# Kernel optimization log

Measured on AMD Instinct MI355X. Metric: run time of the kernel, lower is better.

The kernel has to match this reference:

```python
import jax, jax.numpy as jnp
import numpy as np

D_MODEL = 512
D_K = 64
D_V = 64
N_HEADS = 8
N = 4096
EPS = 1e-5


def setup_inputs() -> dict:
    key = jax.random.key(0)
    ks = jax.random.split(key, 12)
    s = 1.0 / np.sqrt(D_MODEL)
    return {
        "Q": jax.random.normal(ks[0], (N, D_MODEL), dtype=jnp.float32),
        "K": jax.random.normal(ks[1], (N, D_MODEL), dtype=jnp.float32),
        "V": jax.random.normal(ks[2], (N, D_MODEL), dtype=jnp.float32),
        "W_Q": jax.random.normal(ks[3], (D_K * N_HEADS, D_MODEL), dtype=jnp.float32) * s,
        "b_Q": jnp.zeros((D_K * N_HEADS,), jnp.float32),
        "W_K": jax.random.normal(ks[4], (D_K * N_HEADS, D_MODEL), dtype=jnp.float32) * s,
        "b_K": jnp.zeros((D_K * N_HEADS,), jnp.float32),
        "W_V": jax.random.normal(ks[5], (D_V * N_HEADS, D_MODEL), dtype=jnp.float32) * s,
        "b_V": jnp.zeros((D_V * N_HEADS,), jnp.float32),
        "W_O": jax.random.normal(ks[6], (D_MODEL, N_HEADS * D_V), dtype=jnp.float32) * s,
        "b_O": jnp.zeros((D_MODEL,), jnp.float32),
        "gamma": jnp.ones((D_MODEL,), jnp.float32),
        "beta": jnp.zeros((D_MODEL,), jnp.float32),
    }


def reference(Q, K, V, W_Q, b_Q, W_K, b_K, W_V, b_V, W_O, b_O, gamma, beta):
    n = Q.shape[0]
    # projections (torch Linear: x @ W.T + b), then split heads: [N, H, dk]
    Qs = (Q @ W_Q.T + b_Q).reshape(n, N_HEADS, D_K)
    Ks = (K @ W_K.T + b_K).reshape(n, N_HEADS, D_K)
    Vs = (V @ W_V.T + b_V).reshape(n, N_HEADS, D_V)
    # per-head scaled dot-product attention over the N dim, batched via einsum
    scores = jnp.einsum("nhd,mhd->hnm", Qs, Ks) / np.sqrt(D_K)  # [H, N, N]
    attn = jax.nn.softmax(scores, axis=-1)
    ctx = jnp.einsum("hnm,mhd->nhd", attn, Vs)  # [N, H, dv]
    context = ctx.reshape(n, N_HEADS * D_V)  # concat heads (matches torch.cat order)
    out = context @ W_O.T + b_O + Q  # output proj + residual
    # LayerNorm over last dim
    mu = jnp.mean(out, axis=-1, keepdims=True)
    var = jnp.mean((out - mu) ** 2, axis=-1, keepdims=True)
    return (out - mu) * jax.lax.rsqrt(var + EPS) * gamma + beta
```

## Files before the change

### kernel.cpp

```cpp
#include <hip/hip_runtime.h>
#include <cstdint>

#define N_TOK 4096
#define DMODEL 512
#define NHEADS 8
#define HDIM 64

typedef unsigned short u16;
typedef __bf16 bf16x8 __attribute__((ext_vector_type(8)));
typedef float f32x4 __attribute__((ext_vector_type(4)));

union U128 { uint4 u; bf16x8 b; u16 s[8]; };

__device__ __forceinline__ u16 f2bf(float f) {
  uint32_t u = __builtin_bit_cast(uint32_t, f);
  u += 0x7FFFu + ((u >> 16) & 1u);
  return (u16)(u >> 16);
}
__device__ __forceinline__ float bf2f(u16 s) {
  uint32_t u = ((uint32_t)s) << 16;
  return __builtin_bit_cast(float, u);
}
__device__ __forceinline__ uint32_t fbit(float f) { return __builtin_bit_cast(uint32_t, f); }

#if __has_builtin(__builtin_amdgcn_exp2f)
#define EXP2(x) __builtin_amdgcn_exp2f(x)
#else
#define EXP2(x) __expf((x) * 0.6931471805599453f)
#endif

__device__ __forceinline__ void ldg2lds16(const void* g, void* s) {
  __builtin_amdgcn_global_load_lds(
      (const __attribute__((address_space(1))) void*)g,
      (__attribute__((address_space(3))) void*)s, 16, 0, 0);
}

__global__ __launch_bounds__(256) void cvt7_kernel(
    const float* __restrict__ Q, const float* __restrict__ K, const float* __restrict__ V,
    const float* __restrict__ WQ, const float* __restrict__ WK, const float* __restrict__ WV,
    const float* __restrict__ WO,
    u16* __restrict__ Qb, u16* __restrict__ Kb, u16* __restrict__ Vb,
    u16* __restrict__ WQb, u16* __restrict__ WKb, u16* __restrict__ WVb,
    u16* __restrict__ WOb)
{
  int b = blockIdx.x;
  const float* src; u16* dst; int rel;
  if      (b < 2048) { src = Q;  dst = Qb;  rel = b; }
  else if (b < 4096) { src = K;  dst = Kb;  rel = b - 2048; }
  else if (b < 6144) { src = V;  dst = Vb;  rel = b - 4096; }
  else if (b < 6400) { src = WQ; dst = WQb; rel = b - 6144; }
  else if (b < 6656) { src = WK; dst = WKb; rel = b - 6400; }
  else if (b < 6912) { src = WV; dst = WVb; rel = b - 6656; }
  else               { src = WO; dst = WOb; rel = b - 6912; }
  int i = (rel * 256 + threadIdx.x) * 4;
  float4 f = *(const float4*)(src + i);
  ushort4 o;
  o.x = f2bf(f.x); o.y = f2bf(f.y); o.z = f2bf(f.z); o.w = f2bf(f.w);
  *(ushort4*)(dst + i) = o;
}

__global__ __launch_bounds__(256) void proj3_kernel(
    const u16* __restrict__ Qb, const u16* __restrict__ Kb, const u16* __restrict__ Vb,
    const u16* __restrict__ WQb, const u16* __restrict__ WKb, const u16* __restrict__ WVb,
    const float* __restrict__ bQ, const float* __restrict__ bK, const float* __restrict__ bV,
    u16* __restrict__ Qs, u16* __restrict__ Ks, u16* __restrict__ Vt)
{
  const int z = blockIdx.z;
  const u16* A      = (z == 0) ? Qb : (z == 1) ? Kb : Vb;
  const u16* W      = (z == 0) ? WQb : (z == 1) ? WKb : WVb;
  const float* bias = (z == 0) ? bQ : (z == 1) ? bK : bV;

  const int m0 = blockIdx.x * 128;
  const int j0 = blockIdx.y * 64;
  const int tid = threadIdx.x;
  const int w = tid >> 6, lane = tid & 63, quad = lane >> 4, l = lane & 15;

  __shared__ bf16x8 sA[2][8][128];
  __shared__ bf16x8 sB[2][8][64];

  const f32x4 zero = {0.f, 0.f, 0.f, 0.f};
  f32x4 acc[2][4];
#pragma unroll
  for (int m = 0; m < 2; ++m)
#pragma unroll
    for (int s = 0; s < 4; ++s) acc[m][s] = zero;

  auto stage = [&](int kt, int buf) {
    const int k0 = kt * 64;
#pragma unroll
    for (int i = 0; i < 4; ++i) {
      const int chunk = 2 * w + (i >> 1), half = (i & 1) * 64;
      const u16* ag = A + (size_t)(m0 + half + lane) * DMODEL + k0 + chunk * 8;
      ldg2lds16(ag, (char*)&sA[buf][chunk][half]);
    }
#pragma unroll
    for (int i = 0; i < 2; ++i) {
      const int chunk = 2 * w + i;
      const u16* bg = W + (size_t)(j0 + lane) * DMODEL + k0 + chunk * 8;
      ldg2lds16(bg, (char*)&sB[buf][chunk][0]);
    }
  };

  stage(0, 0);
  __syncthreads();
  for (int kt = 0; kt < 8; ++kt) {
    const int buf = kt & 1;
    if (kt + 1 < 8) stage(kt + 1, buf ^ 1);
#pragma unroll
    for (int c = 0; c < 2; ++c) {
      bf16x8 af0 = sA[buf][c * 4 + quad][w * 32 + l];
      bf16x8 af1 = sA[buf][c * 4 + quad][w * 32 + 16 + l];
#pragma unroll
      for (int s = 0; s < 4; ++s) {
        bf16x8 bfb = sB[buf][c * 4 + quad][s * 16 + l];
        acc[0][s] = __builtin_amdgcn_mfma_f32_16x16x32_bf16(af0, bfb, acc[0][s], 0, 0, 0);
        acc[1][s] = __builtin_amdgcn_mfma_f32_16x16x32_bf16(af1, bfb, acc[1][s], 0, 0, 0);
      }
    }
    __syncthreads();
  }

#pragma unroll
  for (int m = 0; m < 2; ++m)
#pragma unroll
    for (int s = 0; s < 4; ++s) {
      int j = j0 + s * 16 + l;
      float bv = bias[j];
      int n0 = m0 + w * 32 + m * 16 + quad * 4;
      if (z < 2) {
        u16* Y = (z == 0) ? Qs : Ks;
#pragma unroll
        for (int r = 0; r < 4; ++r)
          Y[(size_t)(n0 + r) * DMODEL + j] = f2bf(acc[m][s][r] + bv);
      } else {
        ushort4 pk;
        pk.x = f2bf(acc[m][s][0] + bv); pk.y = f2bf(acc[m][s][1] + bv);
        pk.z = f2bf(acc[m][s][2] + bv); pk.w = f2bf(acc[m][s][3] + bv);
        *(ushort4*)(Vt + (size_t)j * N_TOK + n0) = pk;
      }
    }
}

__global__ __launch_bounds__(512, 4) void attn_kernel(
    const u16* __restrict__ Qs, const u16* __restrict__ Ks,
    const u16* __restrict__ Vt, u16* __restrict__ Opart, float* __restrict__ Lpart)
{
  const int hs = blockIdx.x;
  const int h = hs & 7, split = hs >> 3;
  const int qt = blockIdx.y;
  const int tid = threadIdx.x;
  const int w = tid >> 6, lane = tid & 63, quad = lane >> 4, l = lane & 15;

  __shared__ bf16x8 kch[2][8][64];
  __shared__ bf16x8 vch[2][8][64];
  __shared__ __align__(16) u16 pbuf[8][32][40];

  const int wq0 = qt * 256 + w * 32;

  bf16x8 qf[2][2];
#pragma unroll
  for (int c = 0; c < 2; ++c)
#pragma unroll
    for (int m = 0; m < 2; ++m) {
      U128 u;
      u.u = *(const uint4*)(Qs + (size_t)(wq0 + m * 16 + l) * DMODEL + h * HDIM + c * 32 + quad * 8);
#pragma unroll
      for (int j = 0; j < 8; ++j) u.s[j] = f2bf(bf2f(u.s[j]) * 0.18033688f);
      qf[c][m] = u.b;
    }

  const f32x4 zero = {0.f, 0.f, 0.f, 0.f};
  f32x4 o[2][4];
  float lsum[2] = {0.f, 0.f};
#pragma unroll
  for (int m = 0; m < 2; ++m)
#pragma unroll
    for (int s = 0; s < 4; ++s) o[m][s] = zero;

  auto stage = [&](int it, int buf) {
    const int j0 = split * 1024 + it * 64;
    if (w < 4) {
      const u16* kg = Ks + (size_t)(j0 + lane) * DMODEL + h * HDIM + w * 16;
      ldg2lds16(kg,     (char*)&kch[buf][2 * w][0]);
      ldg2lds16(kg + 8, (char*)&kch[buf][2 * w + 1][0]);
    } else {
      const int w2 = w - 4;
      const u16* vg = Vt + (size_t)(h * HDIM + lane) * N_TOK + j0 + w2 * 16;
      ldg2lds16(vg,     (char*)&vch[buf][2 * w2][0]);
      ldg2lds16(vg + 8, (char*)&vch[buf][2 * w2 + 1][0]);
    }
  };

  stage(0, 0);
  __syncthreads();

  for (int it = 0; it < 16; ++it) {
    const int buf = it & 1;
    if (it + 1 < 16) stage(it + 1, buf ^ 1);

#pragma unroll
    for (int kh = 0; kh < 2; ++kh) {
#pragma unroll
      for (int tt = 0; tt < 2; ++tt) {
        const int t = kh * 2 + tt;
        f32x4 sacc[2];
        sacc[0] = zero; sacc[1] = zero;
#pragma unroll
        for (int c = 0; c < 2; ++c) {
          bf16x8 kf = kch[buf][c * 4 + quad][t * 16 + l];
          sacc[0] = __builtin_amdgcn_mfma_f32_16x16x32_bf16(kf, qf[c][0], sacc[0], 0, 0, 0);
          sacc[1] = __builtin_amdgcn_mfma_f32_16x16x32_bf16(kf, qf[c][1], sacc[1], 0, 0, 0);
        }
#pragma unroll
        for (int m = 0; m < 2; ++m) {
          float p0 = EXP2(sacc[m][0]);
          float p1 = EXP2(sacc[m][1]);
          float p2 = EXP2(sacc[m][2]);
          float p3 = EXP2(sacc[m][3]);
          lsum[m] += (p0 + p1) + (p2 + p3);
          uint2 st;
          st.x = (fbit(p0) >> 16) | (fbit(p1) & 0xFFFF0000u);
          st.y = (fbit(p2) >> 16) | (fbit(p3) & 0xFFFF0000u);
          *(uint2*)&pbuf[w][m * 16 + l][tt * 16 + quad * 4] = st;
        }
      }
      U128 pf0, pf1;
      pf0.u = *(const uint4*)&pbuf[w][l][quad * 8];
      pf1.u = *(const uint4*)&pbuf[w][16 + l][quad * 8];
#pragma unroll
      for (int s = 0; s < 4; ++s) {
        bf16x8 vf = vch[buf][kh * 4 + quad][s * 16 + l];
        o[0][s] = __builtin_amdgcn_mfma_f32_16x16x32_bf16(pf0.b, vf, o[0][s], 0, 0, 0);
        o[1][s] = __builtin_amdgcn_mfma_f32_16x16x32_bf16(pf1.b, vf, o[1][s], 0, 0, 0);
      }
    }
    __syncthreads();
  }

#pragma unroll
  for (int m = 0; m < 2; ++m) {
    lsum[m] += __shfl_xor(lsum[m], 16);
    lsum[m] += __shfl_xor(lsum[m], 32);
  }
  if (quad == 0) {
    Lpart[((size_t)split * NHEADS + h) * N_TOK + wq0 + l]      = lsum[0];
    Lpart[((size_t)split * NHEADS + h) * N_TOK + wq0 + 16 + l] = lsum[1];
  }
  u16* Ob = Opart + ((size_t)(split * NHEADS + h) * N_TOK + wq0) * 64;
#pragma unroll
  for (int m = 0; m < 2; ++m)
#pragma unroll
    for (int s = 0; s < 4; ++s)
#pragma unroll
      for (int r = 0; r < 4; ++r)
        Ob[(size_t)(m * 16 + quad * 4 + r) * 64 + s * 16 + l] = f2bf(o[m][s][r]);
}

__global__ __launch_bounds__(256) void combine_kernel(
    const u16* __restrict__ Opart, const float* __restrict__ Lpart,
    u16* __restrict__ ctx)
{
  int idx = blockIdx.x * 256 + threadIdx.x;
  int n = idx >> 6;
  int c8 = idx & 63;
  int h = c8 >> 3;
  int vd0 = (c8 & 7) * 8;

  float acc[8] = {0, 0, 0, 0, 0, 0, 0, 0};
  float lsum = 0.f;
#pragma unroll
  for (int s = 0; s < 4; ++s) {
    U128 u;
    u.u = *(const uint4*)(Opart + ((size_t)(s * NHEADS + h) * N_TOK + n) * 64 + vd0);
#pragma unroll
    for (int j = 0; j < 8; ++j) acc[j] += bf2f(u.s[j]);
    lsum += Lpart[((size_t)s * NHEADS + h) * N_TOK + n];
  }
  float inv = 1.f / lsum;
  U128 u;
#pragma unroll
  for (int j = 0; j < 8; ++j) u.s[j] = f2bf(acc[j] * inv);
  *(uint4*)(ctx + (size_t)n * DMODEL + h * HDIM + vd0) = u.u;
}

__global__ __launch_bounds__(256) void gemmo_kernel(
    const u16* __restrict__ ctx, const u16* __restrict__ WOb,
    const float* __restrict__ bO, const float* __restrict__ resid,
    float* __restrict__ Y)
{
  const int m0 = blockIdx.x * 64;
  const int j0 = blockIdx.y * 64;
  const int tid = threadIdx.x;
  const int w = tid >> 6, lane = tid & 63, quad = lane >> 4, l = lane & 15;

  __shared__ bf16x8 sA[2][8][64];
  __shared__ bf16x8 sB[2][8][64];

  const f32x4 zero = {0.f, 0.f, 0.f, 0.f};
  f32x4 acc[4];
#pragma unroll
  for (int s = 0; s < 4; ++s) acc[s] = zero;

  auto stage = [&](int kt, int buf) {
    const int k0 = kt * 64;
#pragma unroll
    for (int i = 0; i < 2; ++i) {
      const int chunk = 2 * w + i;
      const u16* ag = ctx + (size_t)(m0 + lane) * DMODEL + k0 + chunk * 8;
      ldg2lds16(ag, (char*)&sA[buf][chunk][0]);
      const u16* bg = WOb + (size_t)(j0 + lane) * DMODEL + k0 + chunk * 8;
      ldg2lds16(bg, (char*)&sB[buf][chunk][0]);
    }
  };

  stage(0, 0);
  __syncthreads();
  for (int kt = 0; kt < 8; ++kt) {
    const int buf = kt & 1;
    if (kt + 1 < 8) stage(kt + 1, buf ^ 1);
#pragma unroll
    for (int c = 0; c < 2; ++c) {
      bf16x8 af = sA[buf][c * 4 + quad][w * 16 + l];
#pragma unroll
      for (int s = 0; s < 4; ++s) {
        bf16x8 bfb = sB[buf][c * 4 + quad][s * 16 + l];
        acc[s] = __builtin_amdgcn_mfma_f32_16x16x32_bf16(af, bfb, acc[s], 0, 0, 0);
      }
    }
    __syncthreads();
  }
#pragma unroll
  for (int s = 0; s < 4; ++s) {
    int j = j0 + s * 16 + l;
    float bv = bO[j];
    int n0 = m0 + w * 16 + quad * 4;
#pragma unroll
    for (int r = 0; r < 4; ++r)
      Y[(size_t)(n0 + r) * DMODEL + j] = acc[s][r] + bv + resid[(size_t)(n0 + r) * DMODEL + j];
  }
}

__global__ __launch_bounds__(256) void ln_kernel(
    const float* __restrict__ X, const float* __restrict__ gamma,
    const float* __restrict__ beta, float* __restrict__ Y)
{
  const int w = threadIdx.x >> 6, lane = threadIdx.x & 63;
  const int row = blockIdx.x * 4 + w;
  const float* x = X + (size_t)row * DMODEL + lane * 8;
  float4 a = *(const float4*)x;
  float4 b = *(const float4*)(x + 4);

  float s = a.x + a.y + a.z + a.w + b.x + b.y + b.z + b.w;
#pragma unroll
  for (int m = 1; m < 64; m <<= 1) s += __shfl_xor(s, m);
  float mu = s * (1.f / DMODEL);

  float d0 = a.x - mu, d1 = a.y - mu, d2 = a.z - mu, d3 = a.w - mu;
  float d4 = b.x - mu, d5 = b.y - mu, d6 = b.z - mu, d7 = b.w - mu;
  float v = d0*d0 + d1*d1 + d2*d2 + d3*d3 + d4*d4 + d5*d5 + d6*d6 + d7*d7;
#pragma unroll
  for (int m = 1; m < 64; m <<= 1) v += __shfl_xor(v, m);
  float sc = rsqrtf(v * (1.f / DMODEL) + 1e-5f);

  const float* g = gamma + lane * 8;
  const float* be = beta + lane * 8;
  float4 go = *(const float4*)g;
  float4 g1 = *(const float4*)(g + 4);
  float4 bo = *(const float4*)be;
  float4 b1 = *(const float4*)(be + 4);

  float4 y0, y1;
  y0.x = d0 * sc * go.x + bo.x;  y0.y = d1 * sc * go.y + bo.y;
  y0.z = d2 * sc * go.z + bo.z;  y0.w = d3 * sc * go.w + bo.w;
  y1.x = d4 * sc * g1.x + b1.x;  y1.y = d5 * sc * g1.y + b1.y;
  y1.z = d6 * sc * g1.z + b1.z;  y1.w = d7 * sc * g1.w + b1.w;

  float* yp = Y + (size_t)row * DMODEL + lane * 8;
  *(float4*)yp = y0;
  *(float4*)(yp + 4) = y1;
}

extern "C" void kernel_launch(void* const* d_in, const int* in_sizes, int n_in,
                              void* d_out, int out_size, void* d_ws, size_t ws_size,
                              hipStream_t stream)
{
  const float* Q     = (const float*)d_in[0];
  const float* K     = (const float*)d_in[1];
  const float* V     = (const float*)d_in[2];
  const float* WQ    = (const float*)d_in[3];
  const float* bQ    = (const float*)d_in[4];
  const float* WK    = (const float*)d_in[5];
  const float* bK    = (const float*)d_in[6];
  const float* WV    = (const float*)d_in[7];
  const float* bV    = (const float*)d_in[8];
  const float* WO    = (const float*)d_in[9];
  const float* bO    = (const float*)d_in[10];
  const float* gamma = (const float*)d_in[11];
  const float* beta  = (const float*)d_in[12];

  const size_t MB = 1ull << 20;
  char* ws = (char*)d_ws;
  u16* Qb   = (u16*)(ws + 0 * MB);
  u16* Kb   = (u16*)(ws + 4 * MB);
  u16* Vb   = (u16*)(ws + 8 * MB);
  u16* WQb  = (u16*)(ws + 12 * MB);
  u16* WKb  = (u16*)(ws + 12 * MB + 512 * 1024);
  u16* WVb  = (u16*)(ws + 13 * MB);
  u16* WOb  = (u16*)(ws + 13 * MB + 512 * 1024);
  u16* Qs   = (u16*)(ws + 14 * MB);
  u16* Ks   = (u16*)(ws + 18 * MB);
  u16* Vt   = (u16*)(ws + 22 * MB);
  u16* ctx  = (u16*)(ws + 26 * MB);
  u16* Opart = (u16*)(ws + 30 * MB);
  float* tmp = (float*)(ws + 30 * MB);
  float* Lpart = (float*)(ws + 46 * MB);
  float* out = (float*)d_out;

  cvt7_kernel<<<7168, 256, 0, stream>>>(Q, K, V, WQ, WK, WV, WO,
                                        Qb, Kb, Vb, WQb, WKb, WVb, WOb);
  proj3_kernel<<<dim3(32, 8, 3), 256, 0, stream>>>(Qb, Kb, Vb, WQb, WKb, WVb,
                                                   bQ, bK, bV, Qs, Ks, Vt);
  attn_kernel<<<dim3(32, 16), 512, 0, stream>>>(Qs, Ks, Vt, Opart, Lpart);
  combine_kernel<<<1024, 256, 0, stream>>>(Opart, Lpart, ctx);
  gemmo_kernel<<<dim3(64, 8), 256, 0, stream>>>(ctx, WOb, bO, Q, tmp);
  ln_kernel<<<1024, 256, 0, stream>>>(tmp, gamma, beta, out);
}
```

Baseline: 181.0 us.

## Fuse split-KV combine and LayerNorm into producers via last-block atomic counters

Removes the separate combine and LayerNorm launches. The last attention block to finish for each (head, query-tile) reduces the four split partials into ctx, and the last output-projection block for each row tile applies LayerNorm to its 64 rows. Each handoff uses threadfence plus an atomic counter, with a memset added to reset the counters. This saves two launches and some global round-trips, but the reduction and LayerNorm tails now run serially on a few blocks while others idle.

```diff
diff --git a/kernel.cpp b/kernel.cpp
--- a/kernel.cpp
+++ b/kernel.cpp
@@ -143,7 +143,8 @@
 
 __global__ __launch_bounds__(512, 4) void attn_kernel(
     const u16* __restrict__ Qs, const u16* __restrict__ Ks,
-    const u16* __restrict__ Vt, u16* __restrict__ Opart, float* __restrict__ Lpart)
+    const u16* __restrict__ Vt, u16* __restrict__ Opart, float* __restrict__ Lpart,
+    u16* __restrict__ ctx, unsigned int* __restrict__ cnt)
 {
   const int hs = blockIdx.x;
   const int h = hs & 7, split = hs >> 3;
@@ -154,6 +155,7 @@
   __shared__ bf16x8 kch[2][8][64];
   __shared__ bf16x8 vch[2][8][64];
   __shared__ __align__(16) u16 pbuf[8][32][40];
+  __shared__ int lastflag;
 
   const int wq0 = qt * 256 + w * 32;
 
@@ -254,39 +256,47 @@
 #pragma unroll
       for (int r = 0; r < 4; ++r)
         Ob[(size_t)(m * 16 + quad * 4 + r) * 64 + s * 16 + l] = f2bf(o[m][s][r]);
-}
-
-__global__ __launch_bounds__(256) void combine_kernel(
-    const u16* __restrict__ Opart, const float* __restrict__ Lpart,
-    u16* __restrict__ ctx)
-{
-  int idx = blockIdx.x * 256 + threadIdx.x;
-  int n = idx >> 6;
-  int c8 = idx & 63;
-  int h = c8 >> 3;
-  int vd0 = (c8 & 7) * 8;
-
-  float acc[8] = {0, 0, 0, 0, 0, 0, 0, 0};
-  float lsum = 0.f;
-#pragma unroll
-  for (int s = 0; s < 4; ++s) {
-    U128 u;
-    u.u = *(const uint4*)(Opart + ((size_t)(s * NHEADS + h) * N_TOK + n) * 64 + vd0);
-#pragma unroll
-    for (int j = 0; j < 8; ++j) acc[j] += bf2f(u.s[j]);
-    lsum += Lpart[((size_t)s * NHEADS + h) * N_TOK + n];
-  }
-  float inv = 1.f / lsum;
-  U128 u;
-#pragma unroll
-  for (int j = 0; j < 8; ++j) u.s[j] = f2bf(acc[j] * inv);
-  *(uint4*)(ctx + (size_t)n * DMODEL + h * HDIM + vd0) = u.u;
+
+  __threadfence();
+  __syncthreads();
+  if (tid == 0) {
+    unsigned int old = atomicAdd(&cnt[h * 16 + qt], 1u);
+    lastflag = (old == 3u);
+  }
+  __syncthreads();
+  if (lastflag) {
+    __threadfence();
+#pragma unroll
+    for (int i = 0; i < 4; ++i) {
+      int flat = tid + 512 * i;
+      int q = flat >> 3;
+      int vd0 = (flat & 7) * 8;
+      int n = qt * 256 + q;
+      float acc[8] = {0, 0, 0, 0, 0, 0, 0, 0};
+      float ls = 0.f;
+#pragma unroll
+      for (int s = 0; s < 4; ++s) {
+        U128 u;
+        u.u = *(const uint4*)(Opart + ((size_t)(s * NHEADS + h) * N_TOK + n) * 64 + vd0);
+#pragma unroll
+        for (int j = 0; j < 8; ++j) acc[j] += bf2f(u.s[j]);
+        ls += Lpart[((size_t)s * NHEADS + h) * N_TOK + n];
+      }
+      float inv = 1.f / ls;
+      U128 o8;
+#pragma unroll
+      for (int j = 0; j < 8; ++j) o8.s[j] = f2bf(acc[j] * inv);
+      *(uint4*)(ctx + (size_t)n * DMODEL + h * HDIM + vd0) = o8.u;
+    }
+  }
 }
 
 __global__ __launch_bounds__(256) void gemmo_kernel(
     const u16* __restrict__ ctx, const u16* __restrict__ WOb,
     const float* __restrict__ bO, const float* __restrict__ resid,
-    float* __restrict__ Y)
+    float* __restrict__ Y,
+    const float* __restrict__ gamma, const float* __restrict__ beta,
+    float* __restrict__ out, unsigned int* __restrict__ cnt2)
 {
   const int m0 = blockIdx.x * 64;
   const int j0 = blockIdx.y * 64;
@@ -295,6 +305,7 @@
 
   __shared__ bf16x8 sA[2][8][64];
   __shared__ bf16x8 sB[2][8][64];
+  __shared__ int lastf;
 
   const f32x4 zero = {0.f, 0.f, 0.f, 0.f};
   f32x4 acc[4];
@@ -338,46 +349,52 @@
     for (int r = 0; r < 4; ++r)
       Y[(size_t)(n0 + r) * DMODEL + j] = acc[s][r] + bv + resid[(size_t)(n0 + r) * DMODEL + j];
   }
-}
-
-__global__ __launch_bounds__(256) void ln_kernel(
-    const float* __restrict__ X, const float* __restrict__ gamma,
-    const float* __restrict__ beta, float* __restrict__ Y)
-{
-  const int w = threadIdx.x >> 6, lane = threadIdx.x & 63;
-  const int row = blockIdx.x * 4 + w;
-  const float* x = X + (size_t)row * DMODEL + lane * 8;
-  float4 a = *(const float4*)x;
-  float4 b = *(const float4*)(x + 4);
-
-  float s = a.x + a.y + a.z + a.w + b.x + b.y + b.z + b.w;
-#pragma unroll
-  for (int m = 1; m < 64; m <<= 1) s += __shfl_xor(s, m);
-  float mu = s * (1.f / DMODEL);
-
-  float d0 = a.x - mu, d1 = a.y - mu, d2 = a.z - mu, d3 = a.w - mu;
-  float d4 = b.x - mu, d5 = b.y - mu, d6 = b.z - mu, d7 = b.w - mu;
-  float v = d0*d0 + d1*d1 + d2*d2 + d3*d3 + d4*d4 + d5*d5 + d6*d6 + d7*d7;
-#pragma unroll
-  for (int m = 1; m < 64; m <<= 1) v += __shfl_xor(v, m);
-  float sc = rsqrtf(v * (1.f / DMODEL) + 1e-5f);
-
-  const float* g = gamma + lane * 8;
-  const float* be = beta + lane * 8;
-  float4 go = *(const float4*)g;
-  float4 g1 = *(const float4*)(g + 4);
-  float4 bo = *(const float4*)be;
-  float4 b1 = *(const float4*)(be + 4);
-
-  float4 y0, y1;
-  y0.x = d0 * sc * go.x + bo.x;  y0.y = d1 * sc * go.y + bo.y;
-  y0.z = d2 * sc * go.z + bo.z;  y0.w = d3 * sc * go.w + bo.w;
-  y1.x = d4 * sc * g1.x + b1.x;  y1.y = d5 * sc * g1.y + b1.y;
-  y1.z = d6 * sc * g1.z + b1.z;  y1.w = d7 * sc * g1.w + b1.w;
-
-  float* yp = Y + (size_t)row * DMODEL + lane * 8;
-  *(float4*)yp = y0;
-  *(float4*)(yp + 4) = y1;
+
+  __threadfence();
+  __syncthreads();
+  if (tid == 0) {
+    unsigned int old = atomicAdd(&cnt2[blockIdx.x], 1u);
+    lastf = (old == 7u);
+  }
+  __syncthreads();
+  if (lastf) {
+    __threadfence();
+    for (int rr = 0; rr < 16; ++rr) {
+      const int row = m0 + w * 16 + rr;
+      const float* x = Y + (size_t)row * DMODEL + lane * 8;
+      float4 a = *(const float4*)x;
+      float4 b = *(const float4*)(x + 4);
+
+      float s = a.x + a.y + a.z + a.w + b.x + b.y + b.z + b.w;
+#pragma unroll
+      for (int m = 1; m < 64; m <<= 1) s += __shfl_xor(s, m);
+      float mu = s * (1.f / DMODEL);
+
+      float d0 = a.x - mu, d1 = a.y - mu, d2 = a.z - mu, d3 = a.w - mu;
+      float d4 = b.x - mu, d5 = b.y - mu, d6 = b.z - mu, d7 = b.w - mu;
+      float v = d0*d0 + d1*d1 + d2*d2 + d3*d3 + d4*d4 + d5*d5 + d6*d6 + d7*d7;
+#pragma unroll
+      for (int m = 1; m < 64; m <<= 1) v += __shfl_xor(v, m);
+      float sc = rsqrtf(v * (1.f / DMODEL) + 1e-5f);
+
+      const float* g = gamma + lane * 8;
+      const float* be = beta + lane * 8;
+      float4 go = *(const float4*)g;
+      float4 g1 = *(const float4*)(g + 4);
+      float4 bo = *(const float4*)be;
+      float4 b1 = *(const float4*)(be + 4);
+
+      float4 y0, y1;
+      y0.x = d0 * sc * go.x + bo.x;  y0.y = d1 * sc * go.y + bo.y;
+      y0.z = d2 * sc * go.z + bo.z;  y0.w = d3 * sc * go.w + bo.w;
+      y1.x = d4 * sc * g1.x + b1.x;  y1.y = d5 * sc * g1.y + b1.y;
+      y1.z = d6 * sc * g1.z + b1.z;  y1.w = d7 * sc * g1.w + b1.w;
+
+      float* yp = out + (size_t)row * DMODEL + lane * 8;
+      *(float4*)yp = y0;
+      *(float4*)(yp + 4) = y1;
+    }
+  }
 }
 
 extern "C" void kernel_launch(void* const* d_in, const int* in_sizes, int n_in,
@@ -414,14 +431,16 @@
   u16* Opart = (u16*)(ws + 30 * MB);
   float* tmp = (float*)(ws + 30 * MB);
   float* Lpart = (float*)(ws + 46 * MB);
+  unsigned int* cnt  = (unsigned int*)(ws + 47 * MB);
+  unsigned int* cnt2 = (unsigned int*)(ws + 47 * MB + 4096);
   float* out = (float*)d_out;
 
+  hipMemsetAsync(cnt, 0, 8192, stream);
   cvt7_kernel<<<7168, 256, 0, stream>>>(Q, K, V, WQ, WK, WV, WO,
                                         Qb, Kb, Vb, WQb, WKb, WVb, WOb);
   proj3_kernel<<<dim3(32, 8, 3), 256, 0, stream>>>(Qb, Kb, Vb, WQb, WKb, WVb,
                                                    bQ, bK, bV, Qs, Ks, Vt);
-  attn_kernel<<<dim3(32, 16), 512, 0, stream>>>(Qs, Ks, Vt, Opart, Lpart);
-  combine_kernel<<<1024, 256, 0, stream>>>(Opart, Lpart, ctx);
-  gemmo_kernel<<<dim3(64, 8), 256, 0, stream>>>(ctx, WOb, bO, Q, tmp);
-  ln_kernel<<<1024, 256, 0, stream>>>(tmp, gamma, beta, out);
-}
+  attn_kernel<<<dim3(32, 16), 512, 0, stream>>>(Qs, Ks, Vt, Opart, Lpart, ctx, cnt);
+  gemmo_kernel<<<dim3(64, 8), 256, 0, stream>>>(ctx, WOb, bO, Q, tmp,
+                                                gamma, beta, out, cnt2);
+}
```

Measured after the change: 425.7 us. +135.2%, slower.

## Fuse output projection GEMM with LayerNorm into a single kernel

Applied to the files above, without the earlier changes.

Merges the output projection GEMM and the LayerNorm kernel so each block computes 16 full rows across all 512 columns and normalizes them in-register using a cross-wave shared-memory reduction. This removes the fp32 intermediate buffer write/read and one kernel launch. In exchange each block reloads the entire W_O matrix, raising L2 traffic, and the grid shrinks to 256 blocks with less reuse per tile; variance now uses the sum-of-squares formula.

```diff
diff --git a/kernel.cpp b/kernel.cpp
--- a/kernel.cpp
+++ b/kernel.cpp
@@ -283,34 +283,42 @@
   *(uint4*)(ctx + (size_t)n * DMODEL + h * HDIM + vd0) = u.u;
 }
 
-__global__ __launch_bounds__(256) void gemmo_kernel(
+__global__ __launch_bounds__(256) void gemmo_ln_kernel(
     const u16* __restrict__ ctx, const u16* __restrict__ WOb,
     const float* __restrict__ bO, const float* __restrict__ resid,
-    float* __restrict__ Y)
-{
-  const int m0 = blockIdx.x * 64;
-  const int j0 = blockIdx.y * 64;
+    const float* __restrict__ gamma, const float* __restrict__ beta,
+    float* __restrict__ out)
+{
+  const int m0 = blockIdx.x * 16;
   const int tid = threadIdx.x;
   const int w = tid >> 6, lane = tid & 63, quad = lane >> 4, l = lane & 15;
 
-  __shared__ bf16x8 sA[2][8][64];
-  __shared__ bf16x8 sB[2][8][64];
+  __shared__ bf16x8 sA[2][8][16];
+  __shared__ bf16x8 sB[2][8][512];
+  __shared__ float redS[4][16], redQ[4][16];
 
   const f32x4 zero = {0.f, 0.f, 0.f, 0.f};
-  f32x4 acc[4];
-#pragma unroll
-  for (int s = 0; s < 4; ++s) acc[s] = zero;
+  f32x4 acc[8];
+#pragma unroll
+  for (int s = 0; s < 8; ++s) acc[s] = zero;
 
   auto stage = [&](int kt, int buf) {
     const int k0 = kt * 64;
-#pragma unroll
-    for (int i = 0; i < 2; ++i) {
-      const int chunk = 2 * w + i;
-      const u16* ag = ctx + (size_t)(m0 + lane) * DMODEL + k0 + chunk * 8;
-      ldg2lds16(ag, (char*)&sA[buf][chunk][0]);
-      const u16* bg = WOb + (size_t)(j0 + lane) * DMODEL + k0 + chunk * 8;
-      ldg2lds16(bg, (char*)&sB[buf][chunk][0]);
-    }
+    if (w == 0) {
+#pragma unroll
+      for (int g = 0; g < 2; ++g) {
+        const u16* ag = ctx + (size_t)(m0 + (lane & 15)) * DMODEL + k0 + (g * 4 + (lane >> 4)) * 8;
+        ldg2lds16(ag, (char*)&sA[buf][g * 4][0]);
+      }
+    }
+#pragma unroll
+    for (int chunk = 0; chunk < 8; ++chunk)
+#pragma unroll
+      for (int jg = 0; jg < 2; ++jg) {
+        const int j = w * 128 + jg * 64 + lane;
+        const u16* bg = WOb + (size_t)j * DMODEL + k0 + chunk * 8;
+        ldg2lds16(bg, (char*)&sB[buf][chunk][w * 128 + jg * 64]);
+      }
   };
 
   stage(0, 0);
@@ -320,64 +328,63 @@
     if (kt + 1 < 8) stage(kt + 1, buf ^ 1);
 #pragma unroll
     for (int c = 0; c < 2; ++c) {
-      bf16x8 af = sA[buf][c * 4 + quad][w * 16 + l];
-#pragma unroll
-      for (int s = 0; s < 4; ++s) {
-        bf16x8 bfb = sB[buf][c * 4 + quad][s * 16 + l];
+      bf16x8 af = sA[buf][c * 4 + quad][l];
+#pragma unroll
+      for (int s = 0; s < 8; ++s) {
+        bf16x8 bfb = sB[buf][c * 4 + quad][w * 128 + s * 16 + l];
         acc[s] = __builtin_amdgcn_mfma_f32_16x16x32_bf16(af, bfb, acc[s], 0, 0, 0);
       }
     }
     __syncthreads();
   }
-#pragma unroll
-  for (int s = 0; s < 4; ++s) {
-    int j = j0 + s * 16 + l;
+
+  float y[8][4];
+  float sum[4] = {0, 0, 0, 0}, sq[4] = {0, 0, 0, 0};
+#pragma unroll
+  for (int s = 0; s < 8; ++s) {
+    int j = w * 128 + s * 16 + l;
     float bv = bO[j];
-    int n0 = m0 + w * 16 + quad * 4;
-#pragma unroll
-    for (int r = 0; r < 4; ++r)
-      Y[(size_t)(n0 + r) * DMODEL + j] = acc[s][r] + bv + resid[(size_t)(n0 + r) * DMODEL + j];
-  }
-}
-
-__global__ __launch_bounds__(256) void ln_kernel(
-    const float* __restrict__ X, const float* __restrict__ gamma,
-    const float* __restrict__ beta, float* __restrict__ Y)
-{
-  const int w = threadIdx.x >> 6, lane = threadIdx.x & 63;
-  const int row = blockIdx.x * 4 + w;
-  const float* x = X + (size_t)row * DMODEL + lane * 8;
-  float4 a = *(const float4*)x;
-  float4 b = *(const float4*)(x + 4);
-
-  float s = a.x + a.y + a.z + a.w + b.x + b.y + b.z + b.w;
-#pragma unroll
-  for (int m = 1; m < 64; m <<= 1) s += __shfl_xor(s, m);
-  float mu = s * (1.f / DMODEL);
-
-  float d0 = a.x - mu, d1 = a.y - mu, d2 = a.z - mu, d3 = a.w - mu;
-  float d4 = b.x - mu, d5 = b.y - mu, d6 = b.z - mu, d7 = b.w - mu;
-  float v = d0*d0 + d1*d1 + d2*d2 + d3*d3 + d4*d4 + d5*d5 + d6*d6 + d7*d7;
-#pragma unroll
-  for (int m = 1; m < 64; m <<= 1) v += __shfl_xor(v, m);
-  float sc = rsqrtf(v * (1.f / DMODEL) + 1e-5f);
-
-  const float* g = gamma + lane * 8;
-  const float* be = beta + lane * 8;
-  float4 go = *(const float4*)g;
-  float4 g1 = *(const float4*)(g + 4);
-  float4 bo = *(const float4*)be;
-  float4 b1 = *(const float4*)(be + 4);
-
-  float4 y0, y1;
-  y0.x = d0 * sc * go.x + bo.x;  y0.y = d1 * sc * go.y + bo.y;
-  y0.z = d2 * sc * go.z + bo.z;  y0.w = d3 * sc * go.w + bo.w;
-  y1.x = d4 * sc * g1.x + b1.x;  y1.y = d5 * sc * g1.y + b1.y;
-  y1.z = d6 * sc * g1.z + b1.z;  y1.w = d7 * sc * g1.w + b1.w;
-
-  float* yp = Y + (size_t)row * DMODEL + lane * 8;
-  *(float4*)yp = y0;
-  *(float4*)(yp + 4) = y1;
+#pragma unroll
+    for (int r = 0; r < 4; ++r) {
+      int n = m0 + quad * 4 + r;
+      float v = acc[s][r] + bv + resid[(size_t)n * DMODEL + j];
+      y[s][r] = v;
+      sum[r] += v;
+      sq[r] += v * v;
+    }
+  }
+#pragma unroll
+  for (int r = 0; r < 4; ++r) {
+#pragma unroll
+    for (int m = 1; m < 16; m <<= 1) {
+      sum[r] += __shfl_xor(sum[r], m);
+      sq[r]  += __shfl_xor(sq[r], m);
+    }
+  }
+  if (l == 0) {
+#pragma unroll
+    for (int r = 0; r < 4; ++r) {
+      redS[w][quad * 4 + r] = sum[r];
+      redQ[w][quad * 4 + r] = sq[r];
+    }
+  }
+  __syncthreads();
+
+#pragma unroll
+  for (int r = 0; r < 4; ++r) {
+    int row = quad * 4 + r;
+    float ts = redS[0][row] + redS[1][row] + redS[2][row] + redS[3][row];
+    float tq = redQ[0][row] + redQ[1][row] + redQ[2][row] + redQ[3][row];
+    float mu = ts * (1.f / DMODEL);
+    float var = tq * (1.f / DMODEL) - mu * mu;
+    float sc = rsqrtf(var + 1e-5f);
+    int n = m0 + row;
+#pragma unroll
+    for (int s = 0; s < 8; ++s) {
+      int j = w * 128 + s * 16 + l;
+      out[(size_t)n * DMODEL + j] = (y[s][r] - mu) * sc * gamma[j] + beta[j];
+    }
+  }
 }
 
 extern "C" void kernel_launch(void* const* d_in, const int* in_sizes, int n_in,
@@ -412,7 +419,6 @@
   u16* Vt   = (u16*)(ws + 22 * MB);
   u16* ctx  = (u16*)(ws + 26 * MB);
   u16* Opart = (u16*)(ws + 30 * MB);
-  float* tmp = (float*)(ws + 30 * MB);
   float* Lpart = (float*)(ws + 46 * MB);
   float* out = (float*)d_out;
 
@@ -422,6 +428,5 @@
                                                    bQ, bK, bV, Qs, Ks, Vt);
   attn_kernel<<<dim3(32, 16), 512, 0, stream>>>(Qs, Ks, Vt, Opart, Lpart);
   combine_kernel<<<1024, 256, 0, stream>>>(Opart, Lpart, ctx);
-  gemmo_kernel<<<dim3(64, 8), 256, 0, stream>>>(ctx, WOb, bO, Q, tmp);
-  ln_kernel<<<1024, 256, 0, stream>>>(tmp, gamma, beta, out);
-}
+  gemmo_ln_kernel<<<256, 256, 0, stream>>>(ctx, WOb, bO, Q, gamma, beta, out);
+}
```

After: 200.7 us. 1.11x slower.
